# Kernel optimization log

Measured on AMD Instinct MI355X. Metric: run time of the kernel, lower is better.

Reference implementation:

```python
import jax, jax.numpy as jnp
import numpy as np

EMB_DIM = 2048
N_HEADS = 16
HEAD_DIM = EMB_DIM // N_HEADS
B, S = 4, 2048


def setup_inputs() -> dict:
    key = jax.random.key(0)
    kx, kq, kk, kv, ko = jax.random.split(key, 5)
    scale = 0.02
    return {
        "x": jax.random.normal(kx, (B, S, EMB_DIM), dtype=jnp.float32),
        "Wq": jax.random.normal(kq, (EMB_DIM, EMB_DIM), dtype=jnp.float32) * scale,
        "Wk": jax.random.normal(kk, (EMB_DIM, EMB_DIM), dtype=jnp.float32) * scale,
        "Wv": jax.random.normal(kv, (EMB_DIM, EMB_DIM), dtype=jnp.float32) * scale,
        "Wo": jax.random.normal(ko, (EMB_DIM, EMB_DIM), dtype=jnp.float32) * scale,
        "bo": jnp.zeros((EMB_DIM,), dtype=jnp.float32),
    }


def _split_heads(t):
    # [B, S, E] -> [B, H, S, Dh]
    b, s, _ = t.shape
    return t.reshape(b, s, N_HEADS, HEAD_DIM).transpose(0, 2, 1, 3)


def reference(x, Wq, Wk, Wv, Wo, bo):
    # torch nn.Linear: y = x @ W.T (no bias for qkv, bias for out_proj)
    q = _split_heads(x @ Wq.T)  # [B, H, S, Dh]
    k = _split_heads(x @ Wk.T)
    v = _split_heads(x @ Wv.T)

    scores = jnp.einsum("bhqd,bhkd->bhqk", q, k)  # [B, H, S, S]
    q_pos = jnp.arange(S)
    k_pos = jnp.arange(S)
    causal_mask = q_pos[:, None] < k_pos[None, :]  # True => future token, masked
    scores = jnp.where(causal_mask, -jnp.inf, scores)
    attn = jax.nn.softmax(scores / np.sqrt(HEAD_DIM).astype(np.float32), axis=-1)
    # dropout rate 0 (eval) -> identity
    ctx = jnp.einsum("bhqk,bhkd->bhqd", attn, v)  # [B, H, S, Dh]
    ctx = ctx.transpose(0, 2, 1, 3).reshape(B, S, EMB_DIM)
    return ctx @ Wo.T + bo
```

## Files before the change

### kernel.cpp

```cpp
#include <hip/hip_runtime.h>
#include <math.h>

#define EMB 2048
#define HD 128
#define SEQ 2048
#define MTOT 8192

typedef __bf16 bf16x8 __attribute__((ext_vector_type(8)));
typedef float floatx4 __attribute__((ext_vector_type(4)));

__device__ __forceinline__ unsigned short f2bf(float f) {
    unsigned u = __float_as_uint(f);
    return (unsigned short)((u + 0x7FFFu + ((u >> 16) & 1u)) >> 16);
}

__device__ __forceinline__ void gl_lds16(const void* g, void* lds) {
    __builtin_amdgcn_global_load_lds(
        (const __attribute__((address_space(1))) unsigned int*)g,
        (__attribute__((address_space(3))) unsigned int*)lds,
        16, 0, 0);
}

__global__ void cast_all_kernel(const float* __restrict__ x,
                                const float* __restrict__ w0,
                                const float* __restrict__ w1,
                                const float* __restrict__ w2,
                                const float* __restrict__ w3,
                                unsigned short* __restrict__ xb,
                                unsigned short* __restrict__ wb0,
                                unsigned short* __restrict__ wb1,
                                unsigned short* __restrict__ wb2,
                                unsigned short* __restrict__ wb3)
{
    const int XN4 = MTOT * EMB / 4;
    const int WN4 = EMB * EMB / 4;
    int i = blockIdx.x * blockDim.x + threadIdx.x;
    const float* src; unsigned short* dst; int off;
    if (i < XN4) { src = x; dst = xb; off = i; }
    else {
        int j = i - XN4;
        int wsel = j >> 20;
        off = j & (WN4 - 1);
        switch (wsel) {
            case 0: src = w0; dst = wb0; break;
            case 1: src = w1; dst = wb1; break;
            case 2: src = w2; dst = wb2; break;
            default: src = w3; dst = wb3; break;
        }
    }
    float4 v = reinterpret_cast<const float4*>(src)[off];
    ushort4 o;
    o.x = f2bf(v.x); o.y = f2bf(v.y); o.z = f2bf(v.z); o.w = f2bf(v.w);
    reinterpret_cast<ushort4*>(dst)[off] = o;
}


#define PH_PRE()  do { asm volatile("s_barrier" ::: "memory");               \
                       asm volatile("s_waitcnt lgkmcnt(0)" ::: "memory");    \
                       __builtin_amdgcn_sched_barrier(0);                    \
                       __builtin_amdgcn_s_setprio(1); } while (0)
#define PH_POST() do { __builtin_amdgcn_s_setprio(0);                        \
                       asm volatile("s_barrier" ::: "memory"); } while (0)

#define MFMA16(AF, BF, MI0)                                                  \
    _Pragma("unroll")                                                        \
    for (int mi = 0; mi < 4; mi++)                                           \
        _Pragma("unroll")                                                    \
        for (int ni = 0; ni < 4; ni++)                                       \
            acc[(MI0) + mi][ni] = __builtin_amdgcn_mfma_f32_16x16x32_bf16(   \
                AF[(MI0) + mi], BF[ni], acc[(MI0) + mi][ni], 0, 0, 0);

#define KTILE(BUF, S1, S2, S3, S4, VM)                                       \
  do {                                                                       \
    bf16x8 a0[8], b0[4];                                                     \
    _Pragma("unroll")                                                        \
    for (int mi = 0; mi < 8; mi++)                                           \
        a0[mi] = *reinterpret_cast<const bf16x8*>(baA[BUF][0] + mi * 2048);  \
    _Pragma("unroll")                                                        \
    for (int ni = 0; ni < 4; ni++)                                           \
        b0[ni] = *reinterpret_cast<const bf16x8*>(baB[BUF][0] + ni * 2048);  \
    STAGE(S1);                                                               \
    asm volatile("s_waitcnt lgkmcnt(8)" ::: "memory");                       \
    PH_PRE();                                                                \
    MFMA16(a0, b0, 0);                                                       \
    PH_POST();                                                               \
    bf16x8 a1[8];                                                            \
    _Pragma("unroll")                                                        \
    for (int mi = 0; mi < 8; mi++)                                           \
        a1[mi] = *reinterpret_cast<const bf16x8*>(baA[BUF][1] + mi * 2048);  \
    STAGE(S2);                                                               \
    PH_PRE();                                                                \
    MFMA16(a0, b0, 4);                                                       \
    PH_POST();                                                               \
    bf16x8 b1[4];                                                            \
    _Pragma("unroll")                                                        \
    for (int ni = 0; ni < 4; ni++)                                           \
        b1[ni] = *reinterpret_cast<const bf16x8*>(baB[BUF][1] + ni * 2048);  \
    STAGE(S3);                                                               \
    PH_PRE();                                                                \
    MFMA16(a1, b1, 0);                                                       \
    PH_POST();                                                               \
    STAGE(S4);                                                               \
    asm volatile("s_waitcnt " VM ::: "memory");                              \
    PH_PRE();                                                                \
    MFMA16(a1, b1, 4);                                                       \
    PH_POST();                                                               \
  } while (0)

template<bool OUT_F32>
__global__ __launch_bounds__(512, 2)
void gemm256_bt(const unsigned short* __restrict__ A,
                const unsigned short* __restrict__ Bw0,
                const unsigned short* __restrict__ Bw1,
                const unsigned short* __restrict__ Bw2,
                void* __restrict__ Cout0,
                void* __restrict__ Cout1,
                void* __restrict__ Cout2,
                const float* __restrict__ bias,
                int M, int N, int K, float scale0)
{
    __shared__ __align__(16) unsigned short sA[2][256][64];
    __shared__ __align__(16) unsigned short sB[2][256][64];

    const unsigned short* Bw = (blockIdx.z == 0) ? Bw0 : (blockIdx.z == 1) ? Bw1 : Bw2;
    void* Cout = (blockIdx.z == 0) ? Cout0 : (blockIdx.z == 1) ? Cout1 : Cout2;
    const float osc = (blockIdx.z == 0) ? scale0 : 1.0f;

    const int tid  = threadIdx.x;
    const int lane = tid & 63;
    const int wave = tid >> 6;
    const int wm   = wave >> 2;
    const int wn   = wave & 3;
    const int col  = lane & 15;
    const int quad = lane >> 4;

    int bx = blockIdx.x, by = blockIdx.y;
    {
        int lin = by * 8 + bx;
        int xcd = lin & 7, k = lin >> 3;
        bx = k & 7;
        by = xcd + ((k >> 3) << 3);
    }

    const int m0 = by * 256;
    const int n0 = bx * 256;

    const int NT    = K >> 6;
    const int NITER = NT >> 1;

    int off[2];
    #pragma unroll
    for (int q = 0; q < 2; q++) {
        int P = (tid + (q << 9)) << 4;
        int r = P >> 7;
        int c = ((P & 127) ^ ((r & 7) << 4)) >> 1;
        off[q] = r * K + c;
    }

    const int X = (col & 7) << 4;
    const char* baA[2][2];
    const char* baB[2][2];
    #pragma unroll
    for (int buf = 0; buf < 2; buf++)
        #pragma unroll
        for (int kk = 0; kk < 2; kk++) {
            int sw = (((kk << 6) | (quad << 4)) ^ X);
            baA[buf][kk] = (const char*)&sA[buf][0][0] + (wm << 14) + (col << 7) + sw;
            baB[buf][kk] = (const char*)&sB[buf][0][0] + (wn << 13) + (col << 7) + sw;
        }

    floatx4 acc[8][4];
    #pragma unroll
    for (int i = 0; i < 8; i++)
        #pragma unroll
        for (int j = 0; j < 4; j++)
            #pragma unroll
            for (int r = 0; r < 4; r++) acc[i][j][r] = 0.0f;

    auto STAGE = [&](int s) {
        if (s >= (NT << 2)) return;
        int t = s >> 2, j = s & 3;
        int buf = t & 1;
        int k0 = t << 6;
        int jrow = (j & 1) << 7;
        const unsigned short* src = (j < 2) ? A : Bw;
        int urow = ((j < 2) ? m0 : n0) + jrow;
        const unsigned short* gp = src + (size_t)urow * K + k0;
        unsigned short* region = (j < 2) ? &sA[buf][jrow][0] : &sB[buf][jrow][0];
        char* ldsb = (char*)region + (wave << 10);
        #pragma unroll
        for (int q = 0; q < 2; q++)
            gl_lds16(gp + off[q], ldsb + (q << 13));
    };

    #pragma unroll
    for (int s = 0; s < 6; s++) STAGE(s);
    asm volatile("s_waitcnt vmcnt(4)" ::: "memory");
    asm volatile("s_barrier" ::: "memory");

    #pragma unroll 1
    for (int it = 0; it < NITER - 1; ++it) {
        const int sb = 5 + (it << 3);
        KTILE(0, sb + 1, sb + 2, sb + 3, sb + 4, "vmcnt(4)");
        KTILE(1, sb + 5, sb + 6, sb + 7, sb + 8, "vmcnt(4)");
    }
    {
        const int sb = 5 + ((NITER - 1) << 3);
        KTILE(0, sb + 1, sb + 2, sb + 3, sb + 4, "vmcnt(0)");
        KTILE(1, sb + 5, sb + 6, sb + 7, sb + 8, "vmcnt(4)");
    }

    #pragma unroll
    for (int mi = 0; mi < 8; mi++) {
        #pragma unroll
        for (int ni = 0; ni < 4; ni++) {
            #pragma unroll
            for (int r = 0; r < 4; r++) {
                int row = m0 + (wm << 7) + (mi << 4) + (quad << 2) + r;
                int cg  = n0 + (wn << 6) + (ni << 4) + col;
                float v = acc[mi][ni][r];
                if (OUT_F32) {
                    float bb = bias ? bias[cg] : 0.0f;
                    reinterpret_cast<float*>(Cout)[(size_t)row * N + cg] = v + bb;
                } else {
                    reinterpret_cast<unsigned short*>(Cout)[(size_t)row * N + cg] = f2bf(v * osc);
                }
            }
        }
    }
}

__global__ __launch_bounds__(256, 2)
void flash_attn(const unsigned short* __restrict__ Q,
                const unsigned short* __restrict__ Kg,
                const unsigned short* __restrict__ Vg,
                unsigned short* __restrict__ O)
{
    __shared__ __align__(16) unsigned short sK[2][64 * 128];
    __shared__ __align__(16) unsigned short sVt[2][128][72];
    __shared__ __align__(16) unsigned short sP[4][16 * 72];

    const int tid  = threadIdx.x;
    const int lane = tid & 63;
    const int w    = tid >> 6;
    const int col  = lane & 15;
    const int quad = lane >> 4;

    const int h = blockIdx.y;
    const int b = blockIdx.z;
    const size_t rowbase = (size_t)b * SEQ;
    const int hoff = h * HD;

    unsigned short* sPw = sP[w];

    const int vk4 = (tid & 15) * 4;
    const int vd0 = (tid >> 4) * 8;

    auto stageK = [&](int kt, int buf) {
        const int k0 = kt * 64;
        #pragma unroll
        for (int i = 0; i < 4; i++) {
            int c = tid + i * 256;
            int key = c >> 4;
            int dblk = (c & 15) ^ (key & 7);
            char* ldsK = (char*)sK[buf] + (size_t)(i * 256 + w * 64) * 16;
            gl_lds16(Kg + (rowbase + k0 + key) * EMB + hoff + dblk * 8, ldsK);
        }
    };
    auto loadV = [&](int kt, unsigned short (&va)[4][8]) {
        const int k0 = kt * 64;
        #pragma unroll
        for (int kk = 0; kk < 4; kk++)
            *reinterpret_cast<int4*>(va[kk]) =
                *reinterpret_cast<const int4*>(Vg + (rowbase + k0 + vk4 + kk) * EMB + hoff + vd0);
    };
    auto writeV = [&](unsigned short (&va)[4][8], int buf) {
        #pragma unroll
        for (int j = 0; j < 8; j++) {
            ushort4 o;
            o.x = va[0][j]; o.y = va[1][j]; o.z = va[2][j]; o.w = va[3][j];
            *reinterpret_cast<ushort4*>(&sVt[buf][vd0 + j][vk4]) = o;
        }
    };

    #pragma unroll
    for (int phase = 0; phase < 2; phase++) {
        const int qsb = phase ? (int)blockIdx.x : (SEQ/128 - 1) - (int)blockIdx.x;
        const int qbase = qsb * 128;
        const int qg0 = qbase + w*32 + col;
        const int qg1 = qg0 + 16;

        bf16x8 qf[2][4];
        {
            const unsigned short* qr0 = Q + (rowbase + qg0) * EMB + hoff;
            const unsigned short* qr1 = Q + (rowbase + qg1) * EMB + hoff;
            #pragma unroll
            for (int ks = 0; ks < 4; ks++) {
                qf[0][ks] = *reinterpret_cast<const bf16x8*>(qr0 + ks*32 + quad*8);
                qf[1][ks] = *reinterpret_cast<const bf16x8*>(qr1 + ks*32 + quad*8);
            }
        }

        floatx4 oacc[2][8];
        #pragma unroll
        for (int g = 0; g < 2; g++)
            #pragma unroll
            for (int ni = 0; ni < 8; ni++)
                #pragma unroll
                for (int r = 0; r < 4; r++) oacc[g][ni][r] = 0.0f;
        float l_i[2] = {0.0f, 0.0f};

        const int ktmax = qbase / 64 + 1;

        {
            unsigned short va[4][8];
            stageK(0, 0);
            loadV(0, va);
            writeV(va, 0);
            __syncthreads();
        }

        for (int kt = 0; kt <= ktmax; kt++) {
            const int k0 = kt * 64;
            const int cur = kt & 1;
            const bool have_next = (kt < ktmax);
            unsigned short va[4][8];
            if (have_next) { stageK(kt + 1, cur ^ 1); loadV(kt + 1, va); }

            if (k0 <= qbase + w*32 + 31) {
                floatx4 sc[2][4];
                #pragma unroll
                for (int g = 0; g < 2; g++)
                    #pragma unroll
                    for (int ni = 0; ni < 4; ni++)
                        #pragma unroll
                        for (int r = 0; r < 4; r++) sc[g][ni][r] = 0.0f;
                #pragma unroll
                for (int ni = 0; ni < 4; ni++) {
                    #pragma unroll
                    for (int ks = 0; ks < 4; ks++) {
                        int u = (ni*16 + col) * 16 + ((ks*4 + quad) ^ (col & 7));
                        bf16x8 kf = *reinterpret_cast<const bf16x8*>(&sK[cur][u * 8]);
                        sc[0][ni] = __builtin_amdgcn_mfma_f32_16x16x32_bf16(kf, qf[0][ks], sc[0][ni], 0, 0, 0);
                        sc[1][ni] = __builtin_amdgcn_mfma_f32_16x16x32_bf16(kf, qf[1][ks], sc[1][ni], 0, 0, 0);
                    }
                }

                const bool need_mask = (k0 + 63 > qbase + w*32);
                bf16x8 pf[2][2];

                #pragma unroll
                for (int g = 0; g < 2; g++) {
                    const int qg = (g == 0) ? qg0 : qg1;
                    if (need_mask) {
                        #pragma unroll
                        for (int ni = 0; ni < 4; ni++)
                            #pragma unroll
                            for (int r = 0; r < 4; r++) {
                                int key = k0 + ni*16 + quad*4 + r;
                                if (key > qg) sc[g][ni][r] = -1e30f;
                            }
                    }
                    float rsum = 0.0f;
                    #pragma unroll
                    for (int ni = 0; ni < 4; ni++) {
                        float p0 = __expf(sc[g][ni][0]);
                        float p1 = __expf(sc[g][ni][1]);
                        float p2 = __expf(sc[g][ni][2]);
                        float p3 = __expf(sc[g][ni][3]);
                        rsum += (p0 + p1) + (p2 + p3);
                        ushort4 pk;
                        pk.x = f2bf(p0); pk.y = f2bf(p1); pk.z = f2bf(p2); pk.w = f2bf(p3);
                        *reinterpret_cast<ushort4*>(&sPw[col*72 + ni*16 + quad*4]) = pk;
                    }
                    l_i[g] += rsum;
                    #pragma unroll
                    for (int ks = 0; ks < 2; ks++)
                        pf[g][ks] = *reinterpret_cast<const bf16x8*>(&sPw[col*72 + ks*32 + quad*8]);
                }

                #pragma unroll
                for (int ni = 0; ni < 8; ni++) {
                    #pragma unroll
                    for (int ks = 0; ks < 2; ks++) {
                        bf16x8 vf = *reinterpret_cast<const bf16x8*>(&sVt[cur][ni*16 + col][ks*32 + quad*8]);
                        oacc[0][ni] = __builtin_amdgcn_mfma_f32_16x16x32_bf16(vf, pf[0][ks], oacc[0][ni], 0, 0, 0);
                        oacc[1][ni] = __builtin_amdgcn_mfma_f32_16x16x32_bf16(vf, pf[1][ks], oacc[1][ni], 0, 0, 0);
                    }
                }
            }

            if (have_next) writeV(va, cur ^ 1);
            __syncthreads();
        }

        #pragma unroll
        for (int g = 0; g < 2; g++) {
            const int qg = (g == 0) ? qg0 : qg1;
            float l = l_i[g];
            l += __shfl_xor(l, 16);
            l += __shfl_xor(l, 32);
            float inv = 1.0f / l;
            #pragma unroll
            for (int ni = 0; ni < 8; ni++) {
                ushort4 o4;
                o4.x = f2bf(oacc[g][ni][0] * inv);
                o4.y = f2bf(oacc[g][ni][1] * inv);
                o4.z = f2bf(oacc[g][ni][2] * inv);
                o4.w = f2bf(oacc[g][ni][3] * inv);
                *reinterpret_cast<ushort4*>(O + (rowbase + qg) * EMB + hoff + ni*16 + quad*4) = o4;
            }
        }
    }
}

extern "C" void kernel_launch(void* const* d_in, const int* in_sizes, int n_in,
                              void* d_out, int out_size, void* d_ws, size_t ws_size,
                              hipStream_t stream)
{
    const float* x  = (const float*)d_in[0];
    const float* Wq = (const float*)d_in[1];
    const float* Wk = (const float*)d_in[2];
    const float* Wv = (const float*)d_in[3];
    const float* Wo = (const float*)d_in[4];
    const float* bo = (const float*)d_in[5];
    float* out = (float*)d_out;

    unsigned short* ws = (unsigned short*)d_ws;
    const size_t XN = (size_t)MTOT * EMB;
    const size_t WN = (size_t)EMB * EMB;
    unsigned short* xb  = ws;
    unsigned short* wqb = xb  + XN;
    unsigned short* wkb = wqb + WN;
    unsigned short* wvb = wkb + WN;
    unsigned short* wob = wvb + WN;
    unsigned short* qb  = wob + WN;
    unsigned short* kb  = qb  + XN;
    unsigned short* vb  = kb  + XN;
    unsigned short* ctx = xb;

    {
        int total4 = (int)(XN/4 + 4*(WN/4));
        cast_all_kernel<<<total4 / 256, 256, 0, stream>>>(
            x, Wq, Wk, Wv, Wo, xb, wqb, wkb, wvb, wob);
    }

    const float scl = 0.08838834764831845f;
    gemm256_bt<false><<<dim3(EMB/256, MTOT/256, 3), 512, 0, stream>>>(
        xb, wqb, wkb, wvb, qb, kb, vb, nullptr, MTOT, EMB, EMB, scl);

    flash_attn<<<dim3(SEQ/128/2, 16, 4), 256, 0, stream>>>(qb, kb, vb, ctx);

    gemm256_bt<true><<<dim3(EMB/256, MTOT/256, 1), 512, 0, stream>>>(
        ctx, wob, nullptr, nullptr, out, nullptr, nullptr, bo, MTOT, EMB, EMB, 1.0f);
}
```

Baseline: 575.3 us.

## Restructure GEMM main loop into register double-buffered ping-pong pipeline

Replaces the four-phase KTILE schedule, which had fine-grained per-quarter global staging and two barriers per MFMA phase, with a two-register-set ping-pong. Each set holds one k-half of the LDS fragments, and LDS reads for the next half are issued before the MFMAs on the current half. Global-to-LDS staging is now issued as one whole k-tile per step, followed by a full vmcnt(0) wait. The goal is fewer barriers and better overlap of LDS reads with MFMA. The trade-offs are higher register pressure from two fragment sets and a shallower global prefetch depth, since the full vmcnt(0) wait may expose memory latency.

```diff
diff --git a/kernel.cpp b/kernel.cpp
--- a/kernel.cpp
+++ b/kernel.cpp
@@ -55,12 +55,11 @@
 }
 
 
-#define PH_PRE()  do { asm volatile("s_barrier" ::: "memory");               \
-                       asm volatile("s_waitcnt lgkmcnt(0)" ::: "memory");    \
-                       __builtin_amdgcn_sched_barrier(0);                    \
-                       __builtin_amdgcn_s_setprio(1); } while (0)
-#define PH_POST() do { __builtin_amdgcn_s_setprio(0);                        \
-                       asm volatile("s_barrier" ::: "memory"); } while (0)
+#define BAR()   asm volatile("s_barrier" ::: "memory")
+#define VM0()   asm volatile("s_waitcnt vmcnt(0)" ::: "memory")
+#define SCHED0() __builtin_amdgcn_sched_barrier(0)
+#define PRIO1() __builtin_amdgcn_s_setprio(1)
+#define PRIO0() __builtin_amdgcn_s_setprio(0)
 
 #define MFMA16(AF, BF, MI0)                                                  \
     _Pragma("unroll")                                                        \
@@ -70,41 +69,16 @@
             acc[(MI0) + mi][ni] = __builtin_amdgcn_mfma_f32_16x16x32_bf16(   \
                 AF[(MI0) + mi], BF[ni], acc[(MI0) + mi][ni], 0, 0, 0);
 
-#define KTILE(BUF, S1, S2, S3, S4, VM)                                       \
+#define MFMA32(AF, BF) do { MFMA16(AF, BF, 0); MFMA16(AF, BF, 4); } while (0)
+
+#define READS(SA, SB, BUF, KK)                                               \
   do {                                                                       \
-    bf16x8 a0[8], b0[4];                                                     \
     _Pragma("unroll")                                                        \
     for (int mi = 0; mi < 8; mi++)                                           \
-        a0[mi] = *reinterpret_cast<const bf16x8*>(baA[BUF][0] + mi * 2048);  \
+        SA[mi] = *reinterpret_cast<const bf16x8*>(baA[BUF][KK] + mi * 2048); \
     _Pragma("unroll")                                                        \
     for (int ni = 0; ni < 4; ni++)                                           \
-        b0[ni] = *reinterpret_cast<const bf16x8*>(baB[BUF][0] + ni * 2048);  \
-    STAGE(S1);                                                               \
-    asm volatile("s_waitcnt lgkmcnt(8)" ::: "memory");                       \
-    PH_PRE();                                                                \
-    MFMA16(a0, b0, 0);                                                       \
-    PH_POST();                                                               \
-    bf16x8 a1[8];                                                            \
-    _Pragma("unroll")                                                        \
-    for (int mi = 0; mi < 8; mi++)                                           \
-        a1[mi] = *reinterpret_cast<const bf16x8*>(baA[BUF][1] + mi * 2048);  \
-    STAGE(S2);                                                               \
-    PH_PRE();                                                                \
-    MFMA16(a0, b0, 4);                                                       \
-    PH_POST();                                                               \
-    bf16x8 b1[4];                                                            \
-    _Pragma("unroll")                                                        \
-    for (int ni = 0; ni < 4; ni++)                                           \
-        b1[ni] = *reinterpret_cast<const bf16x8*>(baB[BUF][1] + ni * 2048);  \
-    STAGE(S3);                                                               \
-    PH_PRE();                                                                \
-    MFMA16(a1, b1, 0);                                                       \
-    PH_POST();                                                               \
-    STAGE(S4);                                                               \
-    asm volatile("s_waitcnt " VM ::: "memory");                              \
-    PH_PRE();                                                                \
-    MFMA16(a1, b1, 4);                                                       \
-    PH_POST();                                                               \
+        SB[ni] = *reinterpret_cast<const bf16x8*>(baB[BUF][KK] + ni * 2048); \
   } while (0)
 
 template<bool OUT_F32>
@@ -177,37 +151,72 @@
             #pragma unroll
             for (int r = 0; r < 4; r++) acc[i][j][r] = 0.0f;
 
-    auto STAGE = [&](int s) {
-        if (s >= (NT << 2)) return;
-        int t = s >> 2, j = s & 3;
-        int buf = t & 1;
-        int k0 = t << 6;
-        int jrow = (j & 1) << 7;
-        const unsigned short* src = (j < 2) ? A : Bw;
-        int urow = ((j < 2) ? m0 : n0) + jrow;
-        const unsigned short* gp = src + (size_t)urow * K + k0;
-        unsigned short* region = (j < 2) ? &sA[buf][jrow][0] : &sB[buf][jrow][0];
-        char* ldsb = (char*)region + (wave << 10);
-        #pragma unroll
-        for (int q = 0; q < 2; q++)
-            gl_lds16(gp + off[q], ldsb + (q << 13));
+    auto STAGE_T = [&](int t) {
+        const int bufo = (t & 1) << 15;
+        const int k0   = t << 6;
+        #pragma unroll
+        for (int j = 0; j < 4; j++) {
+            const unsigned short* src = (j < 2) ? A : Bw;
+            const int urow = ((j < 2) ? m0 : n0) + ((j & 1) << 7);
+            const unsigned short* gp = src + (size_t)urow * K + k0;
+            char* ldsb = ((j < 2) ? (char*)sA : (char*)sB)
+                         + bufo + ((j & 1) << 14) + (wave << 10);
+            #pragma unroll
+            for (int q = 0; q < 2; q++)
+                gl_lds16(gp + off[q], ldsb + (q << 13));
+        }
     };
 
-    #pragma unroll
-    for (int s = 0; s < 6; s++) STAGE(s);
-    asm volatile("s_waitcnt vmcnt(4)" ::: "memory");
-    asm volatile("s_barrier" ::: "memory");
+    bf16x8 s0a[8], s0b[4], s1a[8], s1b[4];
+
+    STAGE_T(0);
+    VM0();
+    BAR();
+    READS(s0a, s0b, 0, 0);
 
     #pragma unroll 1
     for (int it = 0; it < NITER - 1; ++it) {
-        const int sb = 5 + (it << 3);
-        KTILE(0, sb + 1, sb + 2, sb + 3, sb + 4, "vmcnt(4)");
-        KTILE(1, sb + 5, sb + 6, sb + 7, sb + 8, "vmcnt(4)");
-    }
+        READS(s1a, s1b, 0, 1);
+        BAR();
+        STAGE_T(2 * it + 1);
+        SCHED0();
+        PRIO1(); MFMA32(s0a, s0b); PRIO0();
+        VM0();
+        BAR();
+        READS(s0a, s0b, 1, 0);
+        SCHED0();
+        PRIO1(); MFMA32(s1a, s1b); PRIO0();
+
+        READS(s1a, s1b, 1, 1);
+        BAR();
+        STAGE_T(2 * it + 2);
+        SCHED0();
+        PRIO1(); MFMA32(s0a, s0b); PRIO0();
+        VM0();
+        BAR();
+        READS(s0a, s0b, 0, 0);
+        SCHED0();
+        PRIO1(); MFMA32(s1a, s1b); PRIO0();
+    }
+
     {
-        const int sb = 5 + ((NITER - 1) << 3);
-        KTILE(0, sb + 1, sb + 2, sb + 3, sb + 4, "vmcnt(0)");
-        KTILE(1, sb + 5, sb + 6, sb + 7, sb + 8, "vmcnt(4)");
+        READS(s1a, s1b, 0, 1);
+        BAR();
+        STAGE_T(NT - 1);
+        SCHED0();
+        PRIO1(); MFMA32(s0a, s0b); PRIO0();
+        VM0();
+        BAR();
+        READS(s0a, s0b, 1, 0);
+        SCHED0();
+        PRIO1(); MFMA32(s1a, s1b); PRIO0();
+
+        READS(s1a, s1b, 1, 1);
+        BAR();
+        SCHED0();
+        PRIO1(); MFMA32(s0a, s0b); PRIO0();
+        SCHED0();
+        PRIO1(); MFMA32(s1a, s1b); PRIO0();
     }
 
     #pragma unroll
```

New measurement: 658.9 us. +14.5%, slower.
